# Optimization experiments

Hardware: AMD Instinct MI355X
Metric: run time of the kernel (lower is better)

Reference implementation:

```python
import jax, jax.numpy as jnp
import numpy as np

BATCH = 4
N_CTX = 1024
D_IN = 512
N_HEADS = 8
D_HEAD = 64
N_VARS = D_IN // D_HEAD  # ConstrainedRead default: n_vars = d_in // d_var = 8
TEMP = 1.0
ATTN_TEMP = float(np.sqrt(D_HEAD))  # attention_temp default = sqrt(d_head)


def setup_inputs() -> dict:
    key = jax.random.key(0)
    k1, k2, k3, k4, k5 = jax.random.split(key, 5)
    x = jax.random.uniform(k1, (BATCH, N_CTX, D_IN), dtype=jnp.float32)
    # causal tril mask, broadcast to batch (matches registered tril buffer usage)
    mask = jnp.broadcast_to(jnp.tril(jnp.ones((N_CTX, N_CTX), dtype=bool)), (BATCH, N_CTX, N_CTX))
    inv_sv = 1.0 / np.sqrt(N_VARS)
    W_K_W = jax.random.normal(k2, (N_HEADS, N_VARS), dtype=jnp.float32) * inv_sv
    W_Q_W = jax.random.normal(k3, (N_HEADS, N_VARS), dtype=jnp.float32) * inv_sv
    W_V_W = jax.random.normal(k4, (N_HEADS, N_VARS), dtype=jnp.float32) * inv_sv
    W_pred_W = jax.random.normal(k5, (N_HEADS, D_HEAD, D_HEAD), dtype=jnp.float32) / np.sqrt(D_HEAD)
    return {"x": x, "mask": mask, "W_K_W": W_K_W, "W_Q_W": W_Q_W, "W_V_W": W_V_W, "W_pred_W": W_pred_W}


def _constrained_read(W):
    # softmax over variables, then block-diagonal-style selector: (h, d_head, d_in)
    probs = jax.nn.softmax(W / TEMP, axis=-1)                 # (h, n_vars)
    eye = jnp.eye(D_HEAD, dtype=probs.dtype)                  # (c, c)
    rm = probs[:, :, None, None] * eye                        # (h, v, c, c)
    # einops 'a b c d -> a d (b c)'
    return jnp.transpose(rm, (0, 3, 1, 2)).reshape(N_HEADS, D_HEAD, D_IN)


def _fixed_bias_table():
    M = N_CTX  # table layout: [-2, linspace(0,-M,M-1)/M, linspace(-M,0,M)/M], shared over heads
    return jnp.concatenate([
        jnp.array([-2.0], dtype=jnp.float32),
        (jnp.linspace(0.0, -float(M), M - 1) / M).astype(jnp.float32),
        (jnp.linspace(-float(M), 0.0, M) / M).astype(jnp.float32),
    ])  # (2M,)


def reference(x, mask, W_K_W, W_Q_W, W_V_W, W_pred_W):
    WK = _constrained_read(W_K_W)
    WQm = _constrained_read(W_Q_W)
    WV = _constrained_read(W_V_W)
    # WPred: out[h,f,d] = sum_e W_Q[h,e,d] * softmax(W)[h,e,f]
    Wp = jax.nn.softmax(W_pred_W / TEMP, axis=-1)
    WQ = jnp.einsum('hed,hef->hfd', WQm, Wp)

    k = jnp.einsum('ihd,bpd->biph', WK, x)   # (b,h,p,dh)
    q = jnp.einsum('ihd,bpd->biph', WQ, x)
    v = jnp.einsum('ihd,bpd->biph', WV, x)

    pre = jnp.einsum('biph,biqh->biqp', k, q)            # (b,h,q,p)
    m = mask[:, None]                                    # (b,1,q,p)
    srow = jnp.where(m, pre, 0.0).sum(-1)                # (b,h,q)
    max_score = srow / (srow + 1e-10)
    pre = pre.at[:, :, :, 0].add(jax.nn.relu(1.0 - max_score))

    nq, nk = pre.shape[-2], pre.shape[-1]
    # relative position gather; %(2M) reproduces torch negative-index wraparound
    rel = (jnp.arange(nk)[None, :] - jnp.arange(nq)[:, None]) % (2 * N_CTX)
    bias = _fixed_bias_table()[rel]                      # (nq,nk), identical per head

    # one_hot_input=True: log(scores + 1e-20) + bias
    pos = jnp.log(pre + 1e-20) + bias[None, None]
    masked = jnp.where(m, pos, -1e30)
    attn = jax.nn.softmax(masked / ATTN_TEMP / TEMP, axis=-1)

    z = jnp.einsum('biph,biqp->biqh', v, attn)           # (b,h,q,dh)
    # einops 'b i q h -> b q (i h)'
    return jnp.transpose(z, (0, 2, 1, 3)).reshape(x.shape[0], nq, N_HEADS * D_HEAD)
```

## Files before the change

kernel.cpp:

```cpp
#include <hip/hip_runtime.h>
#include <math.h>

#define NCTX 1024
#define DIN 512
#define NH 8
#define DH 64

typedef float f32x16 __attribute__((ext_vector_type(16)));
typedef short bf16x8 __attribute__((ext_vector_type(8)));
typedef int i32x4 __attribute__((ext_vector_type(4)));

#define QF_OFF 0
#define KF_OFF (4u * 1024u * 1024u)
#define VF_OFF (8u * 1024u * 1024u)
#define V0_OFF (12u * 1024u * 1024u)

__device__ __forceinline__ bf16x8 asbf(i32x4 v) {
  union { i32x4 i; bf16x8 h; } u;
  u.i = v;
  return u.h;
}

__device__ __forceinline__ bf16x8 mk8(unsigned a, unsigned b, unsigned c,
                                      unsigned d) {
  union { unsigned u[4]; bf16x8 h; } x;
  x.u[0] = a; x.u[1] = b; x.u[2] = c; x.u[3] = d;
  return x.h;
}

__device__ __forceinline__ unsigned cvtpk(float lo, float hi_) {
  unsigned r;
  asm("v_cvt_pk_bf16_f32 %0, %1, %2" : "=v"(r) : "v"(lo), "v"(hi_));
  return r;
}

__device__ __forceinline__ void softmax8(const float* __restrict__ w,
                                         float* __restrict__ p) {
  float mx = w[0];
#pragma unroll
  for (int v = 1; v < 8; ++v) mx = fmaxf(mx, w[v]);
  float s = 0.f;
#pragma unroll
  for (int v = 0; v < 8; ++v) { p[v] = expf(w[v] - mx); s += p[v]; }
  const float inv = 1.f / s;
#pragma unroll
  for (int v = 0; v < 8; ++v) p[v] *= inv;
}

__global__ __launch_bounds__(256) void prep_kernel(
    const float* __restrict__ x, const float* __restrict__ WKw,
    const float* __restrict__ WQw, const float* __restrict__ WVw,
    const float* __restrict__ Wpred, short* __restrict__ Qf,
    short* __restrict__ Kf, short* __restrict__ Vf, float* __restrict__ V0f) {
  const int t = blockIdx.x, ih = blockIdx.y, b = blockIdx.z;
  const int bi = b * NH + ih;
  const int tid = threadIdx.x;

  __shared__ alignas(16) char smem[5 * 8192];
  char* const Ksb = smem;
  char* const Vtb = smem + 8192;
  char* const Q0b = smem + 16384;
  char* const WpT = smem + 24576;
  char* const Qsb = smem + 32768;

  {
    const int e = tid >> 2, sg = tid & 3;
    const float* wr = Wpred + (size_t)(ih * 64 + e) * 64 + sg * 16;
    float e16[16];
    float mx = -1e30f;
#pragma unroll
    for (int j = 0; j < 16; ++j) { e16[j] = wr[j]; mx = fmaxf(mx, e16[j]); }
    mx = fmaxf(mx, __shfl_xor(mx, 1, 4));
    mx = fmaxf(mx, __shfl_xor(mx, 2, 4));
    float s = 0.f;
#pragma unroll
    for (int j = 0; j < 16; ++j) { e16[j] = __expf(e16[j] - mx); s += e16[j]; }
    s += __shfl_xor(s, 1, 4);
    s += __shfl_xor(s, 2, 4);
    const float inv = 1.f / s;
#pragma unroll
    for (int j = 0; j < 16; ++j) {
      const int f = sg * 16 + j;
      const unsigned pz = cvtpk(e16[j] * inv, e16[j] * inv);
      *(unsigned short*)&WpT[f * 128 + ((2 * e) ^ ((f & 7) << 4))] =
          (unsigned short)pz;
    }
  }

  float pk[8], pq8[8], pv[8];
  {
    float w[8];
#pragma unroll
    for (int v = 0; v < 8; ++v) w[v] = WKw[ih * 8 + v];
    softmax8(w, pk);
#pragma unroll
    for (int v = 0; v < 8; ++v) w[v] = WQw[ih * 8 + v];
    softmax8(w, pq8);
#pragma unroll
    for (int v = 0; v < 8; ++v) w[v] = WVw[ih * 8 + v];
    softmax8(w, pv);
  }

  const int rg = tid >> 4, eg = tid & 15;
  const int r0 = rg * 4, e0 = eg * 4;
  float ka[4][4], qa[4][4], va[4][4];
#pragma unroll
  for (int i2 = 0; i2 < 4; ++i2)
#pragma unroll
    for (int j = 0; j < 4; ++j) { ka[i2][j] = 0.f; qa[i2][j] = 0.f; va[i2][j] = 0.f; }

  const float* xb = x + ((size_t)(b * NCTX + t * 64 + r0)) * DIN + e0;
#pragma unroll
  for (int v = 0; v < 8; ++v) {
#pragma unroll
    for (int i2 = 0; i2 < 4; ++i2) {
      const float4 xv = *(const float4*)(xb + (size_t)i2 * DIN + v * 64);
      ka[i2][0] = fmaf(pk[v], xv.x, ka[i2][0]);
      ka[i2][1] = fmaf(pk[v], xv.y, ka[i2][1]);
      ka[i2][2] = fmaf(pk[v], xv.z, ka[i2][2]);
      ka[i2][3] = fmaf(pk[v], xv.w, ka[i2][3]);
      qa[i2][0] = fmaf(pq8[v], xv.x, qa[i2][0]);
      qa[i2][1] = fmaf(pq8[v], xv.y, qa[i2][1]);
      qa[i2][2] = fmaf(pq8[v], xv.z, qa[i2][2]);
      qa[i2][3] = fmaf(pq8[v], xv.w, qa[i2][3]);
      va[i2][0] = fmaf(pv[v], xv.x, va[i2][0]);
      va[i2][1] = fmaf(pv[v], xv.y, va[i2][1]);
      va[i2][2] = fmaf(pv[v], xv.z, va[i2][2]);
      va[i2][3] = fmaf(pv[v], xv.w, va[i2][3]);
    }
  }

  if (t == 0 && rg == 0) {
    *(float4*)(V0f + bi * 64 + e0) =
        make_float4(va[0][0], va[0][1], va[0][2], va[0][3]);
  }

#pragma unroll
  for (int i2 = 0; i2 < 4; ++i2) {
    const int r = r0 + i2;
    const int boff = (2 * e0) ^ ((r & 7) << 4);
    *(uint2*)&Ksb[r * 128 + boff] =
        make_uint2(cvtpk(ka[i2][0], ka[i2][1]), cvtpk(ka[i2][2], ka[i2][3]));
    *(uint2*)&Q0b[r * 128 + boff] =
        make_uint2(cvtpk(qa[i2][0], qa[i2][1]), cvtpk(qa[i2][2], qa[i2][3]));
  }
#pragma unroll
  for (int j = 0; j < 4; ++j) {
    const int rr = e0 + j;
    *(uint2*)&Vtb[rr * 128 + ((2 * r0) ^ ((rr & 7) << 4))] =
        make_uint2(cvtpk(va[0][j], va[1][j]), cvtpk(va[2][j], va[3][j]));
  }
  __syncthreads();

  const int wv = tid >> 6;
  const int l = tid & 63;
  const int lm = l & 31;
  const int hi = l >> 5;

  const size_t fbase = (size_t)bi * 8192 + (size_t)t * 512;
#pragma unroll
  for (int c = 0; c < 2; ++c) {
    const int idx = c * 256 + tid;
    const int pq = idx >> 8, j = (idx >> 6) & 3, ll = idx & 63;
    const int krow = 32 * pq + (ll & 31);
    const i32x4 kfr = *(const i32x4*)
        &Ksb[krow * 128 + ((32 * j + 16 * (ll >> 5)) ^ ((krow & 7) << 4))];
    ((i32x4*)Kf)[fbase + idx] = kfr;
    const int vrow = 32 * (j & 1) + (ll & 31);
    const i32x4 vfr = *(const i32x4*)
        &Vtb[vrow * 128 +
             ((64 * pq + 32 * (j >> 1) + 16 * (ll >> 5)) ^ ((vrow & 7) << 4))];
    ((i32x4*)Vf)[fbase + idx] = vfr;
  }

  {
    const int qq = wv & 1, ff = wv >> 1;
    f32x16 dreg;
#pragma unroll
    for (int r = 0; r < 16; ++r) dreg[r] = 0.f;
    const int arow = 32 * qq + lm;
    const int brow = 32 * ff + lm;
#pragma unroll
    for (int kk = 0; kk < 4; ++kk) {
      const i32x4 af = *(const i32x4*)
          &Q0b[arow * 128 + ((32 * kk + 16 * hi) ^ ((arow & 7) << 4))];
      const i32x4 bfr = *(const i32x4*)
          &WpT[brow * 128 + ((32 * kk + 16 * hi) ^ ((brow & 7) << 4))];
      dreg = __builtin_amdgcn_mfma_f32_32x32x16_bf16(asbf(af), asbf(bfr),
                                                     dreg, 0, 0, 0);
    }
#pragma unroll
    for (int r = 0; r < 16; ++r) {
      const int q = 32 * qq + (r & 3) + 8 * (r >> 2) + 4 * hi;
      const int f = 32 * ff + lm;
      const unsigned pz = cvtpk(dreg[r], dreg[r]);
      *(unsigned short*)&Qsb[q * 128 + ((2 * f) ^ ((q & 7) << 4))] =
          (unsigned short)pz;
    }
  }
  __syncthreads();

#pragma unroll
  for (int c = 0; c < 2; ++c) {
    const int idx = c * 256 + tid;
    const int qq2 = idx >> 8, kk = (idx >> 6) & 3, ll = idx & 63;
    const int row = 32 * qq2 + (ll & 31);
    const i32x4 qfr = *(const i32x4*)
        &Qsb[row * 128 + ((32 * kk + 16 * (ll >> 5)) ^ ((row & 7) << 4))];
    ((i32x4*)Qf)[fbase + idx] = qfr;
  }
}

#if __has_builtin(__builtin_amdgcn_exp2f) && __has_builtin(__builtin_amdgcn_logf)
#define T_LOG(x) __builtin_amdgcn_logf(x)
#define T_EXP(x) __builtin_amdgcn_exp2f(x)
#define T_L 1.7628215e-4f
#define T_DIAG (-0.36067376f)
#else
#define T_LOG(x) __logf(x)
#define T_EXP(x) __expf(x)
#define T_L 1.2219941e-4f
#define T_DIAG (-0.25f)
#endif

__global__ __launch_bounds__(128) void attn_kernel(
    const short* __restrict__ Qf, const short* __restrict__ Kf,
    const short* __restrict__ Vf, const float* __restrict__ V0f,
    float* __restrict__ out) {
  const int bx = blockIdx.x;
  const int a = bx >> 5;
  const int bi = bx & 31;
  const int s = a >> 1;
  const int qhalf = a & 1;
  const int s4 = s >> 2, sm = s & 3;
  const int qt = (s4 == 0) ? (15 - 2 * sm)
               : (s4 == 1) ? (2 * sm)
               : (s4 == 2) ? (14 - 2 * sm)
                           : (2 * sm + 1);
  const int b = bi >> 3, ih = bi & 7;
  const int tid = threadIdx.x;
  const int pq = tid >> 6;
  const int l = tid & 63;
  const int hi = l >> 5;
  const int lm = l & 31;
  const int qq = qhalf;

  __shared__ float num_l[32][64];
  __shared__ float rdn[2][32];
  __shared__ float rsw[2][32];
  __shared__ float rp0[32];
  __shared__ float rdw[32];
  __shared__ float rinv[32];

  const i32x4* Qp = (const i32x4*)Qf + (size_t)bi * 8192 + (size_t)qt * 512 +
                    qq * 256;
  const i32x4* Kp = (const i32x4*)Kf + (size_t)bi * 8192 + pq * 256;
  const i32x4* Vp = (const i32x4*)Vf + (size_t)bi * 8192 + pq * 256;

  bf16x8 qfr[4];
#pragma unroll
  for (int kk = 0; kk < 4; ++kk) qfr[kk] = asbf(Qp[kk * 64 + l]);

  const float v0a = V0f[bi * 64 + lm];
  const float v0b = V0f[bi * 64 + 32 + lm];

  f32x16 num0, num1, stA, stB;
#pragma unroll
  for (int r = 0; r < 16; ++r) { num0[r] = 0.f; num1[r] = 0.f; }
  float den = 0.f, srw = 0.f, pre0 = 0.f;
  const int qg = qt * 64 + 32 * qq + lm;
  const int qpb = qg - 32 * pq - 4 * hi;

  i32x4 kA[4], kB[4], vV[4];

#define LOADK(PT, S)                                                    \
  do {                                                                  \
    const size_t o_ = (size_t)(PT) * 512;                               \
    _Pragma("unroll") for (int kk = 0; kk < 4; ++kk)                    \
        k##S[kk] = Kp[o_ + kk * 64 + l];                                \
  } while (0)

#define LOADV(PT)                                                       \
  do {                                                                  \
    const size_t o_ = (size_t)(PT) * 512;                               \
    _Pragma("unroll") for (int j = 0; j < 4; ++j)                       \
        vV[j] = Vp[o_ + j * 64 + l];                                    \
  } while (0)

#define QKSTEP(S)                                                            \
  do {                                                                       \
    _Pragma("unroll") for (int r = 0; r < 16; ++r) st##S[r] = 0.f;           \
    __builtin_amdgcn_s_setprio(1);                                           \
    _Pragma("unroll") for (int kk = 0; kk < 4; ++kk) st##S =                 \
        __builtin_amdgcn_mfma_f32_32x32x16_bf16(asbf(k##S[kk]), qfr[kk],     \
                                                st##S, 0, 0, 0);             \
    __builtin_amdgcn_s_setprio(0);                                           \
  } while (0)

#define PHASE(PT, CUR, NXT)                                                  \
  do {                                                                       \
    if ((PT) + 1 <= qt) QKSTEP(NXT);                                         \
    if ((PT) + 2 <= qt) LOADK((PT) + 2, CUR);                                \
    const int D0 = qpb - 64 * (PT);                                          \
    const float B0 = (1.0f - (float)D0) * T_L;                               \
    float w_[16];                                                            \
    float d4_[4] = {0.f, 0.f, 0.f, 0.f};                                     \
    if ((PT) == qt) {                              \
      float s4_[4] = {0.f, 0.f, 0.f, 0.f};                                   \
      _Pragma("unroll") for (int r = 0; r < 16; ++r) {                       \
        const int ro = (r & 3) + 8 * (r >> 2);                               \
        const float pre = st##CUR[r];                                        \
        float b2 = B0 + (float)ro * T_L;                                     \
        b2 = (D0 == ro) ? T_DIAG : b2;                                       \
        b2 = (D0 < ro) ? -1e38f : b2;                                        \
        w_[r] = T_EXP(fmaf(0.125f, T_LOG(pre + 1e-20f), b2));                \
        d4_[r & 3] += w_[r];                                                 \
        s4_[r & 3] += (D0 >= ro) ? pre : 0.f;                                \
      }                                                                      \
      srw += (s4_[0] + s4_[1]) + (s4_[2] + s4_[3]);                          \
    } else {                  \
      float s4_[4] = {0.f, 0.f, 0.f, 0.f};                                   \
      _Pragma("unroll") for (int r = 0; r < 16; ++r) {                       \
        const int ro = (r & 3) + 8 * (r >> 2);                               \
        const float pre = st##CUR[r];                                        \
        const float b2 = B0 + (float)ro * T_L;                               \
        w_[r] = T_EXP(fmaf(0.125f, T_LOG(pre + 1e-20f), b2));                \
        d4_[r & 3] += w_[r];                                                 \
        s4_[r & 3] += pre;                                                   \
      }                                                                      \
      srw += (s4_[0] + s4_[1]) + (s4_[2] + s4_[3]);                          \
    }                                                                        \
    den += (d4_[0] + d4_[1]) + (d4_[2] + d4_[3]);                            \
    if ((PT) == 0 && pq == 0 && hi == 0) pre0 = st##CUR[0];                  \
    unsigned P0 = cvtpk(w_[0], w_[1]), P1 = cvtpk(w_[2], w_[3]);             \
    unsigned P2 = cvtpk(w_[4], w_[5]), P3 = cvtpk(w_[6], w_[7]);             \
    unsigned P4 = cvtpk(w_[8], w_[9]), P5 = cvtpk(w_[10], w_[11]);           \
    unsigned P6 = cvtpk(w_[12], w_[13]), P7 = cvtpk(w_[14], w_[15]);         \
    asm("v_permlane32_swap_b32 %0, %1" : "+v"(P0), "+v"(P2));                \
    asm("v_permlane32_swap_b32 %0, %1" : "+v"(P1), "+v"(P3));                \
    asm("v_permlane32_swap_b32 %0, %1" : "+v"(P4), "+v"(P6));                \
    asm("v_permlane32_swap_b32 %0, %1" : "+v"(P5), "+v"(P7));                \
    const bf16x8 wf0 = mk8(P0, P1, P2, P3);                                  \
    const bf16x8 wf1 = mk8(P4, P5, P6, P7);                                  \
    __builtin_amdgcn_s_setprio(1);                                           \
    num0 = __builtin_amdgcn_mfma_f32_32x32x16_bf16(wf0, asbf(vV[0]),         \
                                                   num0, 0, 0, 0);           \
    num1 = __builtin_amdgcn_mfma_f32_32x32x16_bf16(wf0, asbf(vV[1]),         \
                                                   num1, 0, 0, 0);           \
    num0 = __builtin_amdgcn_mfma_f32_32x32x16_bf16(wf1, asbf(vV[2]),         \
                                                   num0, 0, 0, 0);           \
    num1 = __builtin_amdgcn_mfma_f32_32x32x16_bf16(wf1, asbf(vV[3]),         \
                                                   num1, 0, 0, 0);           \
    __builtin_amdgcn_s_setprio(0);                                           \
    if ((PT) + 1 <= qt) LOADV((PT) + 1);                                     \
  } while (0)

  LOADK(0, A);
  if (qt >= 1) LOADK(1, B);
  LOADV(0);
  QKSTEP(A);
  for (int pt = 0; pt <= qt; pt += 2) {
    PHASE(pt, A, B);
    if (pt + 1 > qt) break;
    PHASE(pt + 1, B, A);
  }

  const float dsum = den + __shfl_xor(den, 32, 64);
  const float ssum = srw + __shfl_xor(srw, 32, 64);
  if (hi == 0) {
    rdn[pq][lm] = dsum;
    rsw[pq][lm] = ssum;
    if (pq == 0) rp0[lm] = pre0;
  }
  if (pq == 1) {
#pragma unroll
    for (int r = 0; r < 16; ++r) {
      const int row = (r & 3) + 8 * (r >> 2) + 4 * hi;
      num_l[row][lm] = num0[r];
      num_l[row][32 + lm] = num1[r];
    }
  }
  __syncthreads();
  if (pq == 1 && hi == 0) {
    const int q = lm;
    const float dtot = rdn[0][q] + rdn[1][q];
    const float stot = rsw[0][q] + rsw[1][q];
    const float p0v = rp0[q];
    const float ms = stot / (stot + 1e-10f);
    const float add = fmaxf(1.f - ms, 0.f);
    const int qgq = qt * 64 + qq * 32 + q;
    const float b8 =
        (qgq == 0) ? -0.25f : (1.0f - (float)qgq) * (0.125f / 1023.0f);
    const float w0n = __expf(fmaf(0.125f, __logf(p0v + add + 1e-20f), b8));
    const float w0o = __expf(fmaf(0.125f, __logf(p0v + 1e-20f), b8));
    const float dwv = w0n - w0o;
    rdw[q] = dwv;
    rinv[q] = 1.f / (dtot + dwv);
  }
  __syncthreads();
  if (pq == 0) {
#pragma unroll
    for (int r = 0; r < 16; ++r) {
      const int row = (r & 3) + 8 * (r >> 2) + 4 * hi;
      const int qgq = qt * 64 + qq * 32 + row;
      const float dwv = rdw[row];
      const float iv = rinv[row];
      const float o0 = (num0[r] + num_l[row][lm] + dwv * v0a) * iv;
      const float o1 = (num1[r] + num_l[row][32 + lm] + dwv * v0b) * iv;
      float* op = out + ((size_t)b * NCTX + qgq) * DIN + ih * DH;
      op[lm] = o0;
      op[32 + lm] = o1;
    }
  }
#undef LOADK
#undef LOADV
#undef QKSTEP
#undef PHASE
}

extern "C" void kernel_launch(void* const* d_in, const int* in_sizes, int n_in,
                              void* d_out, int out_size, void* d_ws,
                              size_t ws_size, hipStream_t stream) {
  const float* x = (const float*)d_in[0];
  const float* WKw = (const float*)d_in[2];
  const float* WQw = (const float*)d_in[3];
  const float* WVw = (const float*)d_in[4];
  const float* Wpred = (const float*)d_in[5];
  float* out = (float*)d_out;

  short* Qf = (short*)((char*)d_ws + QF_OFF);
  short* Kf = (short*)((char*)d_ws + KF_OFF);
  short* Vf = (short*)((char*)d_ws + VF_OFF);
  float* V0f = (float*)((char*)d_ws + V0_OFF);

  dim3 block(256);
  dim3 grid1(16, NH, 4);
  hipLaunchKernelGGL(prep_kernel, grid1, block, 0, stream, x, WKw, WQw, WVw,
                     Wpred, Qf, Kf, Vf, V0f);
  dim3 block2(128);
  dim3 grid2(1024);
  hipLaunchKernelGGL(attn_kernel, grid2, block2, 0, stream, Qf, Kf, Vf, V0f,
                     out);
}
```

Baseline: 37.71 us.

## Merge query halves into 256-thread blocks and drop double-buffered score accumulator

Each block now runs four waves covering both 32-row query halves of a 64-row tile, which halves the grid and lets the two halves share K/V loads through cache. The score accumulator is reduced to a single register set, with the next QK MFMA issued only after the current scores are consumed. A waves-per-EU hint of 3 is added. This lowers register pressure to raise occupancy, at the cost of less overlap between the QK MFMA and the exp/log work. The tile ordering is also simplified to a plain descending-then-ascending sequence.

After: 45.46 us. 20.5% more time.

```diff
diff --git a/kernel.cpp b/kernel.cpp
--- a/kernel.cpp
+++ b/kernel.cpp
@@ -223,34 +223,30 @@
 #define T_DIAG (-0.25f)
 #endif
 
-__global__ __launch_bounds__(128) void attn_kernel(
+__global__ __launch_bounds__(256) __attribute__((amdgpu_waves_per_eu(3)))
+void attn_kernel(
     const short* __restrict__ Qf, const short* __restrict__ Kf,
     const short* __restrict__ Vf, const float* __restrict__ V0f,
     float* __restrict__ out) {
   const int bx = blockIdx.x;
   const int a = bx >> 5;
   const int bi = bx & 31;
-  const int s = a >> 1;
-  const int qhalf = a & 1;
-  const int s4 = s >> 2, sm = s & 3;
-  const int qt = (s4 == 0) ? (15 - 2 * sm)
-               : (s4 == 1) ? (2 * sm)
-               : (s4 == 2) ? (14 - 2 * sm)
-                           : (2 * sm + 1);
+  const int qt = (a < 8) ? (15 - a) : (a - 8);
   const int b = bi >> 3, ih = bi & 7;
   const int tid = threadIdx.x;
-  const int pq = tid >> 6;
+  const int wv = tid >> 6;
   const int l = tid & 63;
   const int hi = l >> 5;
   const int lm = l & 31;
-  const int qq = qhalf;
-
-  __shared__ float num_l[32][64];
-  __shared__ float rdn[2][32];
-  __shared__ float rsw[2][32];
-  __shared__ float rp0[32];
-  __shared__ float rdw[32];
-  __shared__ float rinv[32];
+  const int pq = wv & 1;
+  const int qq = wv >> 1;
+
+  __shared__ float num_l[2][32][64];
+  __shared__ float rdn[2][2][32];
+  __shared__ float rsw[2][2][32];
+  __shared__ float rp0[2][32];
+  __shared__ float rdw[2][32];
+  __shared__ float rinv[2][32];
 
   const i32x4* Qp = (const i32x4*)Qf + (size_t)bi * 8192 + (size_t)qt * 512 +
                     qq * 256;
@@ -264,7 +260,7 @@
   const float v0a = V0f[bi * 64 + lm];
   const float v0b = V0f[bi * 64 + 32 + lm];
 
-  f32x16 num0, num1, stA, stB;
+  f32x16 num0, num1, st;
 #pragma unroll
   for (int r = 0; r < 16; ++r) { num0[r] = 0.f; num1[r] = 0.f; }
   float den = 0.f, srw = 0.f, pre0 = 0.f;
@@ -289,18 +285,16 @@
 
 #define QKSTEP(S)                                                            \
   do {                                                                       \
-    _Pragma("unroll") for (int r = 0; r < 16; ++r) st##S[r] = 0.f;           \
+    _Pragma("unroll") for (int r = 0; r < 16; ++r) st[r] = 0.f;              \
     __builtin_amdgcn_s_setprio(1);                                           \
-    _Pragma("unroll") for (int kk = 0; kk < 4; ++kk) st##S =                 \
+    _Pragma("unroll") for (int kk = 0; kk < 4; ++kk) st =                    \
         __builtin_amdgcn_mfma_f32_32x32x16_bf16(asbf(k##S[kk]), qfr[kk],     \
-                                                st##S, 0, 0, 0);             \
+                                                st, 0, 0, 0);                \
     __builtin_amdgcn_s_setprio(0);                                           \
   } while (0)
 
 #define PHASE(PT, CUR, NXT)                                                  \
   do {                                                                       \
-    if ((PT) + 1 <= qt) QKSTEP(NXT);                                         \
-    if ((PT) + 2 <= qt) LOADK((PT) + 2, CUR);                                \
     const int D0 = qpb - 64 * (PT);                                          \
     const float B0 = (1.0f - (float)D0) * T_L;                               \
     float w_[16];                                                            \
@@ -309,7 +303,7 @@
       float s4_[4] = {0.f, 0.f, 0.f, 0.f};                                   \
       _Pragma("unroll") for (int r = 0; r < 16; ++r) {                       \
         const int ro = (r & 3) + 8 * (r >> 2);                               \
-        const float pre = st##CUR[r];                                        \
+        const float pre = st[r];                                             \
         float b2 = B0 + (float)ro * T_L;                                     \
         b2 = (D0 == ro) ? T_DIAG : b2;                                       \
         b2 = (D0 < ro) ? -1e38f : b2;                                        \
@@ -322,7 +316,7 @@
       float s4_[4] = {0.f, 0.f, 0.f, 0.f};                                   \
       _Pragma("unroll") for (int r = 0; r < 16; ++r) {                       \
         const int ro = (r & 3) + 8 * (r >> 2);                               \
-        const float pre = st##CUR[r];                                        \
+        const float pre = st[r];                                             \
         const float b2 = B0 + (float)ro * T_L;                               \
         w_[r] = T_EXP(fmaf(0.125f, T_LOG(pre + 1e-20f), b2));                \
         d4_[r & 3] += w_[r];                                                 \
@@ -331,7 +325,9 @@
       srw += (s4_[0] + s4_[1]) + (s4_[2] + s4_[3]);                          \
     }                                                                        \
     den += (d4_[0] + d4_[1]) + (d4_[2] + d4_[3]);                            \
-    if ((PT) == 0 && pq == 0 && hi == 0) pre0 = st##CUR[0];                  \
+    if ((PT) == 0 && pq == 0 && hi == 0) pre0 = st[0];                       \
+    if ((PT) + 1 <= qt) QKSTEP(NXT);                                         \
+    if ((PT) + 2 <= qt) LOADK((PT) + 2, CUR);                                \
     unsigned P0 = cvtpk(w_[0], w_[1]), P1 = cvtpk(w_[2], w_[3]);             \
     unsigned P2 = cvtpk(w_[4], w_[5]), P3 = cvtpk(w_[6], w_[7]);             \
     unsigned P4 = cvtpk(w_[8], w_[9]), P5 = cvtpk(w_[10], w_[11]);           \
@@ -368,24 +364,24 @@
   const float dsum = den + __shfl_xor(den, 32, 64);
   const float ssum = srw + __shfl_xor(srw, 32, 64);
   if (hi == 0) {
-    rdn[pq][lm] = dsum;
-    rsw[pq][lm] = ssum;
-    if (pq == 0) rp0[lm] = pre0;
+    rdn[qq][pq][lm] = dsum;
+    rsw[qq][pq][lm] = ssum;
+    if (pq == 0) rp0[qq][lm] = pre0;
   }
   if (pq == 1) {
 #pragma unroll
     for (int r = 0; r < 16; ++r) {
       const int row = (r & 3) + 8 * (r >> 2) + 4 * hi;
-      num_l[row][lm] = num0[r];
-      num_l[row][32 + lm] = num1[r];
+      num_l[qq][row][lm] = num0[r];
+      num_l[qq][row][32 + lm] = num1[r];
     }
   }
   __syncthreads();
   if (pq == 1 && hi == 0) {
     const int q = lm;
-    const float dtot = rdn[0][q] + rdn[1][q];
-    const float stot = rsw[0][q] + rsw[1][q];
-    const float p0v = rp0[q];
+    const float dtot = rdn[qq][0][q] + rdn[qq][1][q];
+    const float stot = rsw[qq][0][q] + rsw[qq][1][q];
+    const float p0v = rp0[qq][q];
     const float ms = stot / (stot + 1e-10f);
     const float add = fmaxf(1.f - ms, 0.f);
     const int qgq = qt * 64 + qq * 32 + q;
@@ -394,8 +390,8 @@
     const float w0n = __expf(fmaf(0.125f, __logf(p0v + add + 1e-20f), b8));
     const float w0o = __expf(fmaf(0.125f, __logf(p0v + 1e-20f), b8));
     const float dwv = w0n - w0o;
-    rdw[q] = dwv;
-    rinv[q] = 1.f / (dtot + dwv);
+    rdw[qq][q] = dwv;
+    rinv[qq][q] = 1.f / (dtot + dwv);
   }
   __syncthreads();
   if (pq == 0) {
@@ -403,10 +399,10 @@
     for (int r = 0; r < 16; ++r) {
       const int row = (r & 3) + 8 * (r >> 2) + 4 * hi;
       const int qgq = qt * 64 + qq * 32 + row;
-      const float dwv = rdw[row];
-      const float iv = rinv[row];
-      const float o0 = (num0[r] + num_l[row][lm] + dwv * v0a) * iv;
-      const float o1 = (num1[r] + num_l[row][32 + lm] + dwv * v0b) * iv;
+      const float dwv = rdw[qq][row];
+      const float iv = rinv[qq][row];
+      const float o0 = (num0[r] + num_l[qq][row][lm] + dwv * v0a) * iv;
+      const float o1 = (num1[r] + num_l[qq][row][32 + lm] + dwv * v0b) * iv;
       float* op = out + ((size_t)b * NCTX + qgq) * DIN + ih * DH;
       op[lm] = o0;
       op[32 + lm] = o1;
@@ -437,8 +433,8 @@
   dim3 grid1(16, NH, 4);
   hipLaunchKernelGGL(prep_kernel, grid1, block, 0, stream, x, WKw, WQw, WVw,
                      Wpred, Qf, Kf, Vf, V0f);
-  dim3 block2(128);
-  dim3 grid2(1024);
+  dim3 block2(256);
+  dim3 grid2(512);
   hipLaunchKernelGGL(attn_kernel, grid2, block2, 0, stream, Qf, Kf, Vf, V0f,
                      out);
 }
```
